# Performance work log

Measured on AMD Instinct MI355X. Metric: run time of the kernel, lower is better.

## Reference

```python
import jax, jax.numpy as jnp
import numpy as np
from jax import lax

# static config (matches init_kwargs / input_specs)
B, T, DUR = 16, 256, 4
MEL = T * DUR                      # 1024 frames; durations rows each sum to MEL
D, H, DH, L = 512, 8, 64, 4
INTER, K, OUT = 2048, 3, 80
VOCAB, MAXLEN = 256, 4096


def _sincos(maxlen, d):
    den = jnp.exp(-jnp.arange(0, d, 2).astype(jnp.float32) * (np.log(10000.0) / d))
    ang = jnp.arange(maxlen, dtype=jnp.float32)[:, None] * den[None, :]
    return jnp.stack([jnp.sin(ang), jnp.cos(ang)], axis=-1).reshape(maxlen, d)


def _ln(x, g, b):
    m = jnp.mean(x, -1, keepdims=True)
    v = jnp.mean((x - m) ** 2, -1, keepdims=True)
    return (x - m) * lax.rsqrt(v + 1e-5) * g + b


def _layer(x, am, wqkv, bqkv, wo, bo, ln1g, ln1b, c1w, c1b, c2w, c2b, ln2g, ln2b):
    bs, s, _ = x.shape
    qkv = (x @ wqkv + bqkv).reshape(bs, s, 3, H, DH)
    q, k, v = qkv[:, :, 0], qkv[:, :, 1], qkv[:, :, 2]
    scores = jnp.einsum('bqhd,bkhd->bhqk', q, k) / np.sqrt(DH).astype(np.float32)
    scores = scores + am[:, None, None, :]          # additive key mask (-inf padded)
    attn = jax.nn.softmax(scores, axis=-1)
    ctx = jnp.einsum('bhqk,bkhd->bqhd', attn, v).reshape(bs, s, H * DH)
    x = _ln(x + ctx @ wo + bo, ln1g, ln1b)
    h = lax.conv_general_dilated(x, c1w, (1,), 'SAME', dimension_numbers=('NLC', 'LIO', 'NLC')) + c1b
    h = jax.nn.relu(h)
    h = lax.conv_general_dilated(h, c2w, (1,), 'SAME', dimension_numbers=('NLC', 'LIO', 'NLC')) + c2b
    return _ln(x + h, ln2g, ln2b)


def _stack(x, am, params):
    for i in range(L):
        x = _layer(x, am, *(p[i] for p in params))
    return x


def setup_inputs() -> dict:
    key = jax.random.key(0)
    ks = iter(jax.random.split(key, 64))

    def nrm(shape, s=0.02):
        return jax.random.normal(next(ks), shape, jnp.float32) * s

    inp = {
        'tokens': jax.random.randint(next(ks), (B, T), 0, VOCAB),
        'token_lengths': jax.random.randint(next(ks), (B,), T // 2, T),
        'melspec_length': jax.random.randint(next(ks), (B,), MEL // 2, MEL),
        'durations': jnp.full((B, T), DUR, jnp.int32),   # rows sum to MEL (module assert)
        'mel_len': MEL,
        'emb': nrm((VOCAB, D), 1.0),
    }
    for pre in ('enc', 'dec'):
        inp[pre + '_wqkv'] = nrm((L, D, 3 * H * DH))
        inp[pre + '_bqkv'] = jnp.zeros((L, 3 * H * DH))
        inp[pre + '_wo'] = nrm((L, H * DH, D))
        inp[pre + '_bo'] = jnp.zeros((L, D))
        inp[pre + '_ln1g'] = jnp.ones((L, D))
        inp[pre + '_ln1b'] = jnp.zeros((L, D))
        inp[pre + '_c1w'] = nrm((L, K, D, INTER))
        inp[pre + '_c1b'] = jnp.zeros((L, INTER))
        inp[pre + '_c2w'] = nrm((L, K, INTER, D))
        inp[pre + '_c2b'] = jnp.zeros((L, D))
        inp[pre + '_ln2g'] = jnp.ones((L, D))
        inp[pre + '_ln2b'] = jnp.zeros((L, D))
    inp['out_w'] = nrm((D, OUT))
    inp['out_b'] = jnp.zeros((OUT,))
    return inp


def reference(tokens, token_lengths, melspec_length, durations, mel_len, emb,
              enc_wqkv, enc_bqkv, enc_wo, enc_bo, enc_ln1g, enc_ln1b,
              enc_c1w, enc_c1b, enc_c2w, enc_c2b, enc_ln2g, enc_ln2b,
              dec_wqkv, dec_bqkv, dec_wo, dec_bo, dec_ln1g, dec_ln1b,
              dec_c1w, dec_c1b, dec_c2w, dec_c2b, dec_ln2g, dec_ln2b,
              out_w, out_b):
    bs, t = tokens.shape
    pos = _sincos(MAXLEAN := MAXLEN, D)
    x = emb[tokens]
    # faithful to original: x + (x + pos_embedding[:bs]) where pos buffer is [maxlen,1,D]
    x = 2.0 * x + pos[:bs][:, None, :]
    am = jnp.where(jnp.arange(t)[None, :] > token_lengths[:, None], -jnp.inf, 0.0)
    enc = _stack(x, am, (enc_wqkv, enc_bqkv, enc_wo, enc_bo, enc_ln1g, enc_ln1b,
                         enc_c1w, enc_c1b, enc_c2w, enc_c2b, enc_ln2g, enc_ln2b))
    # length regulator: equivalent gather form of mask.T @ encoder (O(MEL*D) not O(T*MEL*D))
    cums = jnp.cumsum(durations, axis=1)
    frames = jnp.arange(mel_len)
    idx = jax.vmap(lambda c: jnp.searchsorted(c, frames, side='right'))(cums)  # [B, MEL]
    dec_in = jnp.take_along_axis(enc, idx[:, :, None], axis=1)
    keep = (frames[None, :] <= melspec_length[:, None]).astype(dec_in.dtype)
    dec_in = dec_in * keep[:, :, None]
    am2 = jnp.where(frames[None, :] > melspec_length[:, None], -jnp.inf, 0.0)
    dec = _stack(dec_in, am2, (dec_wqkv, dec_bqkv, dec_wo, dec_bo, dec_ln1g, dec_ln1b,
                               dec_c1w, dec_c1b, dec_c2w, dec_c2b, dec_ln2g, dec_ln2b))
    out = dec @ out_w + out_b                      # [B, MEL, OUT]
    return jnp.transpose(out, (0, 2, 1))           # [B, OUT, MEL]
```

## Files before the change

### kernel.cpp

```cpp
#include <hip/hip_runtime.h>

typedef unsigned short u16;
typedef short short8 __attribute__((ext_vector_type(8)));
typedef float floatx4 __attribute__((ext_vector_type(4)));

static constexpr int CB = 16, CT = 256, CMEL = 1024, CD = 512, CH = 8, CDH = 64, CL = 4;
static constexpr int CINTER = 2048, COUT = 80;
static constexpr int CQKV = 3 * CH * CDH;

static __device__ __forceinline__ float bf2f(u16 u) {
  union { unsigned u; float f; } v; v.u = ((unsigned)u) << 16; return v.f;
}
static __device__ __forceinline__ u16 f2bf(float f) {
  union { float f; unsigned u; } v; v.f = f;
  unsigned r = v.u + 0x7fffu + ((v.u >> 16) & 1u);
  return (u16)(r >> 16);
}

static __device__ __forceinline__ void gld16(const u16* g, u16* lds) {
  __builtin_amdgcn_global_load_lds((const __attribute__((address_space(1))) void*)g,
                                   (__attribute__((address_space(3))) void*)lds, 16, 0, 0);
}

template<int NT, bool RELU>
__global__ __launch_bounds__(256)
void gemm2_k(const u16* __restrict__ A, const u16* __restrict__ Bm,
             u16* __restrict__ Cm, const float* __restrict__ bias,
             int M, int N, int K, int lda, int ldb, int ldc,
             int Sm1, long tapStrideB, const u16* __restrict__ zp)
{
  constexpr int BM = 128, BN = 128;
  constexpr int H = (NT == 3) ? 8 : 0;
  constexpr int AR = BM + 2 * H;
  __shared__ u16 As[AR * 32];
  __shared__ u16 Bs[NT * BN * 32];

  const int t = threadIdx.x;
  const int lane = t & 63;
  const int wave = t >> 6;
  const int wrow = wave >> 1;
  const int wcol = wave & 1;
  const int bn0 = blockIdx.x * BN;
  const int bm0 = blockIdx.y * BM;

  floatx4 acc[4][4];
#pragma unroll
  for (int i = 0; i < 4; ++i)
#pragma unroll
    for (int j = 0; j < 4; ++j) acc[i][j] = (floatx4){0.f, 0.f, 0.f, 0.f};

  const int rsub = lane >> 2;
  const int g8 = (((lane & 3) ^ ((lane >> 3) & 3)) << 3);

  const u16* aP0; const u16* aP1; const u16* aP2 = nullptr;
  {
    int gg0 = bm0 - H + wave * 16 + rsub;
    int gg1 = bm0 - H + (wave + 4) * 16 + rsub;
    aP0 = ((NT == 1) || ((unsigned)gg0 < (unsigned)M)) ? A + (long)gg0 * lda + g8 : nullptr;
    aP1 = ((NT == 1) || ((unsigned)gg1 < (unsigned)M)) ? A + (long)gg1 * lda + g8 : nullptr;
    if (NT == 3 && wave == 0) {
      int gg2 = bm0 - H + 128 + rsub;
      aP2 = ((unsigned)gg2 < (unsigned)M) ? A + (long)gg2 * lda + g8 : nullptr;
    }
  }
  const int aL0 = wave * 512, aL1 = (wave + 4) * 512, aL2 = 8 * 512;

  const u16* bP[NT][2]; int bL[NT][2];
#pragma unroll
  for (int i = 0; i < NT; ++i)
#pragma unroll
    for (int j = 0; j < 2; ++j) {
      int r = (wave + j * 4) * 16 + rsub;
      bP[i][j] = Bm + (long)i * tapStrideB + (long)(bn0 + r) * ldb + g8;
      bL[i][j] = (i * BN + (wave + j * 4) * 16) * 32;
    }

  const int q = lane >> 4, fm = lane & 15;
  const int swzB = (q ^ ((fm >> 1) & 3)) << 3;
  int swzA[NT];
  bool mv[NT][4];
#pragma unroll
  for (int tap = 0; tap < NT; ++tap) {
    const int dlt = tap - ((NT == 3) ? 1 : 0);
    swzA[tap] = (q ^ ((((H + dlt + fm) & 15) >> 1) & 3)) << 3;
#pragma unroll
    for (int i = 0; i < 4; ++i) {
      int s = (bm0 + wrow * 64 + i * 16 + fm) & Sm1;
      mv[tap][i] = ((unsigned)(s + dlt) <= (unsigned)Sm1);
    }
  }
  const short8 zero8 = {};

  for (int k0 = 0; k0 < K; k0 += 32) {
    gld16(aP0 ? aP0 + k0 : zp, &As[aL0]);
    gld16(aP1 ? aP1 + k0 : zp, &As[aL1]);
    if (NT == 3 && wave == 0) gld16(aP2 ? aP2 + k0 : zp, &As[aL2]);
#pragma unroll
    for (int i = 0; i < NT; ++i)
#pragma unroll
      for (int j = 0; j < 2; ++j) gld16(bP[i][j] + k0, &Bs[bL[i][j]]);
    __syncthreads();

#pragma unroll
    for (int tap = 0; tap < NT; ++tap) {
      const int dlt = tap - ((NT == 3) ? 1 : 0);
      short8 af[4], bfr[4];
#pragma unroll
      for (int i = 0; i < 4; ++i) {
        af[i] = *(const short8*)&As[(wrow * 64 + i * 16 + fm + H + dlt) * 32 + swzA[tap]];
        if (NT == 3 && !mv[tap][i]) af[i] = zero8;
      }
#pragma unroll
      for (int j = 0; j < 4; ++j)
        bfr[j] = *(const short8*)&Bs[(tap * BN + wcol * 64 + j * 16 + fm) * 32 + swzB];
#pragma unroll
      for (int i = 0; i < 4; ++i)
#pragma unroll
        for (int j = 0; j < 4; ++j)
          acc[i][j] = __builtin_amdgcn_mfma_f32_16x16x32_bf16(af[i], bfr[j], acc[i][j], 0, 0, 0);
    }
    __syncthreads();
  }

  const int rbase = bm0 + wrow * 64 + ((lane >> 4) << 2);
  const int cbase = bn0 + wcol * 64 + fm;
#pragma unroll
  for (int j = 0; j < 4; ++j) {
    int col = cbase + j * 16;
    float bv = bias ? bias[col] : 0.f;
#pragma unroll
    for (int i = 0; i < 4; ++i) {
#pragma unroll
      for (int r = 0; r < 4; ++r) {
        int row = rbase + i * 16 + r;
        float v = acc[i][j][r] + bv;
        if (RELU) v = fmaxf(v, 0.f);
        Cm[(long)row * ldc + col] = f2bf(v);
      }
    }
  }
}

__global__ __launch_bounds__(512)
void attn_k(const u16* __restrict__ qkv, const u16* __restrict__ vt,
            u16* __restrict__ ctx, const int* __restrict__ lens, int S)
{
  __shared__ __attribute__((aligned(16))) u16 Ks[2][128 * 32];
  __shared__ __attribute__((aligned(16))) u16 Vts[4][64 * 32];
  __shared__ __attribute__((aligned(16))) u16 Ps[8][16][136];

  const int t = threadIdx.x, lane = t & 63, w = t >> 6;
  const int bh = blockIdx.y, b = bh >> 3, h = bh & 7;
  const int q0 = blockIdx.x * 128;
  const int len = lens[b];
  const int fm = lane & 15, quad = lane >> 4;
  const int swz8 = ((quad ^ ((fm >> 1) & 3)) << 3);
  const int rsub = lane >> 2;
  const int g8 = (((lane & 3) ^ ((lane >> 3) & 3)) << 3);

  const int qrow = q0 + w * 16 + fm;
  short8 bq[2];
  bq[0] = *(const short8*)&qkv[(long)(b * S + qrow) * CQKV + h * 64 + quad * 8];
  bq[1] = *(const short8*)&qkv[(long)(b * S + qrow) * CQKV + h * 64 + 32 + quad * 8];

  const int ksW = w & 1, rgA = w >> 1, rgB = (w >> 1) + 4;
  const u16* kBaseA = qkv + ((long)b * S + rgA * 16 + rsub) * CQKV + CD + h * 64 + ksW * 32 + g8;
  const u16* kBaseB = qkv + ((long)b * S + rgB * 16 + rsub) * CQKV + CD + h * 64 + ksW * 32 + g8;
  u16* kDstA = &Ks[ksW][rgA * 512];
  u16* kDstB = &Ks[ksW][rgB * 512];
  const int kvs0 = (2 * w) >> 2, dhc0 = (2 * w) & 3;
  const int kvs1 = (2 * w + 1) >> 2, dhc1 = (2 * w + 1) & 3;
  const u16* vBase0 = vt + ((long)bh * 64 + dhc0 * 16 + rsub) * S + kvs0 * 32 + g8;
  const u16* vBase1 = vt + ((long)bh * 64 + dhc1 * 16 + rsub) * S + kvs1 * 32 + g8;
  u16* vDst0 = &Vts[kvs0][dhc0 * 512];
  u16* vDst1 = &Vts[kvs1][dhc1 * 512];

  floatx4 acc_o[4];
#pragma unroll
  for (int j = 0; j < 4; ++j) acc_o[j] = (floatx4){0.f, 0.f, 0.f, 0.f};
  float m = -1e30f, l = 0.f;

  for (int kv0 = 0; kv0 < S; kv0 += 128) {
    __syncthreads();
    gld16(kBaseA + (long)kv0 * CQKV, kDstA);
    gld16(kBaseB + (long)kv0 * CQKV, kDstB);
    gld16(vBase0 + kv0, vDst0);
    gld16(vBase1 + kv0, vDst1);
    __syncthreads();

    floatx4 sa[8];
#pragma unroll
    for (int i = 0; i < 8; ++i) sa[i] = (floatx4){0.f, 0.f, 0.f, 0.f};
#pragma unroll
    for (int ks = 0; ks < 2; ++ks) {
#pragma unroll
      for (int mi = 0; mi < 8; ++mi) {
        short8 ak = *(const short8*)&Ks[ks][(mi * 16 + fm) * 32 + swz8];
        sa[mi] = __builtin_amdgcn_mfma_f32_16x16x32_bf16(ak, bq[ks], sa[mi], 0, 0, 0);
      }
    }

    float p[8][4], tm = -1e30f;
#pragma unroll
    for (int mi = 0; mi < 8; ++mi)
#pragma unroll
      for (int r = 0; r < 4; ++r) {
        int kvg = kv0 + mi * 16 + quad * 4 + r;
        float v = (kvg <= len) ? sa[mi][r] * 0.125f : -1e30f;
        p[mi][r] = v; tm = fmaxf(tm, v);
      }
    tm = fmaxf(tm, __shfl_xor(tm, 16));
    tm = fmaxf(tm, __shfl_xor(tm, 32));
    const float mnew = fmaxf(m, tm);
    const float al = __expf(m - mnew);
    float ts = 0.f;
#pragma unroll
    for (int mi = 0; mi < 8; ++mi)
#pragma unroll
      for (int r = 0; r < 4; ++r) { float e = __expf(p[mi][r] - mnew); p[mi][r] = e; ts += e; }
    ts += __shfl_xor(ts, 16);
    ts += __shfl_xor(ts, 32);
    l = l * al + ts; m = mnew;
    float al4[4];
#pragma unroll
    for (int r = 0; r < 4; ++r) al4[r] = __shfl(al, ((lane >> 4) << 2) + r, 64);
#pragma unroll
    for (int j = 0; j < 4; ++j)
#pragma unroll
      for (int r = 0; r < 4; ++r) acc_o[j][r] *= al4[r];

#pragma unroll
    for (int mi = 0; mi < 8; ++mi) {
      unsigned u01 = (unsigned)f2bf(p[mi][0]) | ((unsigned)f2bf(p[mi][1]) << 16);
      unsigned u23 = (unsigned)f2bf(p[mi][2]) | ((unsigned)f2bf(p[mi][3]) << 16);
      *(uint2*)&Ps[w][fm][mi * 16 + quad * 4] = make_uint2(u01, u23);
    }

#pragma unroll
    for (int kvs = 0; kvs < 4; ++kvs) {
      short8 ap = *(const short8*)&Ps[w][fm][kvs * 32 + quad * 8];
#pragma unroll
      for (int nj = 0; nj < 4; ++nj) {
        short8 bv = *(const short8*)&Vts[kvs][(nj * 16 + fm) * 32 + swz8];
        acc_o[nj] = __builtin_amdgcn_mfma_f32_16x16x32_bf16(ap, bv, acc_o[nj], 0, 0, 0);
      }
    }
  }

  float li4[4];
#pragma unroll
  for (int r = 0; r < 4; ++r) li4[r] = 1.f / __shfl(l, ((lane >> 4) << 2) + r, 64);
#pragma unroll
  for (int nj = 0; nj < 4; ++nj)
#pragma unroll
    for (int r = 0; r < 4; ++r) {
      int qr = q0 + w * 16 + quad * 4 + r;
      ctx[(long)(b * S + qr) * CD + h * 64 + nj * 16 + fm] = f2bf(acc_o[nj][r] * li4[r]);
    }
}

template<int BM, int BN>
__global__ __launch_bounds__(256)
void gemmF_k(const u16* __restrict__ A, const u16* __restrict__ Bm,
             float* __restrict__ Cm, const float* __restrict__ bias,
             int M, int N, int K, int lda, int ldb,
             const u16* __restrict__ zp)
{
  __shared__ u16 As[BM * 32];
  __shared__ u16 Bs[BN * 32];

  const int t = threadIdx.x;
  const int lane = t & 63;
  const int wave = t >> 6;
  constexpr int WCOLS = BN / 64;
  const int wrow = wave / WCOLS;
  const int wcol = wave % WCOLS;
  const int bn0 = blockIdx.x * BN;
  const int bm0 = blockIdx.y * BM;

  floatx4 acc[4][4];
#pragma unroll
  for (int i = 0; i < 4; ++i)
#pragma unroll
    for (int j = 0; j < 4; ++j) acc[i][j] = (floatx4){0.f, 0.f, 0.f, 0.f};

  const int rsub = lane >> 2;
  const int g8 = (((lane & 3) ^ ((lane >> 3) & 3)) << 3);
  constexpr int PA = BM / 64, PB = BN / 64;

  const int q = lane >> 4, fm = lane & 15;
  const int swz8 = ((q ^ ((fm >> 1) & 3)) << 3);

  const u16* aP[PA]; const u16* bP[PB];
#pragma unroll
  for (int p = 0; p < PA; ++p)
    aP[p] = A + (long)(bm0 + p * 64 + wave * 16 + rsub) * lda + g8;
#pragma unroll
  for (int p = 0; p < PB; ++p) {
    int r = p * 64 + wave * 16 + rsub;
    bP[p] = ((bn0 + r) < N) ? (Bm + (long)(bn0 + r) * ldb + g8) : nullptr;
  }

  for (int k0 = 0; k0 < K; k0 += 32) {
#pragma unroll
    for (int p = 0; p < PA; ++p)
      gld16(aP[p] + k0, &As[(p * 64 + wave * 16) * 32]);
#pragma unroll
    for (int p = 0; p < PB; ++p)
      gld16(bP[p] ? bP[p] + k0 : zp, &Bs[(p * 64 + wave * 16) * 32]);
    __syncthreads();

    short8 af[4], bfr[4];
#pragma unroll
    for (int i = 0; i < 4; ++i)
      af[i] = *(const short8*)&As[(wrow * 64 + i * 16 + fm) * 32 + swz8];
#pragma unroll
    for (int j = 0; j < 4; ++j)
      bfr[j] = *(const short8*)&Bs[(wcol * 64 + j * 16 + fm) * 32 + swz8];
#pragma unroll
    for (int i = 0; i < 4; ++i)
#pragma unroll
      for (int j = 0; j < 4; ++j)
        acc[i][j] = __builtin_amdgcn_mfma_f32_16x16x32_bf16(af[i], bfr[j], acc[i][j], 0, 0, 0);
    __syncthreads();
  }

  const int rbase = bm0 + wrow * 64 + ((lane >> 4) << 2);
  const int cbase = bn0 + wcol * 64 + (lane & 15);
#pragma unroll
  for (int j = 0; j < 4; ++j) {
    int col = cbase + j * 16;
    if (col >= N) continue;
    float bv = bias ? bias[col] : 0.f;
#pragma unroll
    for (int i = 0; i < 4; ++i) {
#pragma unroll
      for (int r = 0; r < 4; ++r) {
        int row = rbase + i * 16 + r;
        Cm[((long)(row >> 10) * COUT + col) * CMEL + (row & 1023)] = acc[i][j][r] + bv;
      }
    }
  }
}

__global__ void cvt_t_k(const float* __restrict__ src, u16* __restrict__ dst, int K, int N)
{
  const int tap = blockIdx.z;
  const int n0 = blockIdx.x * 32, k0 = blockIdx.y * 32;
  __shared__ float tile[32][33];
  const int t = threadIdx.x;
  const int c = t & 31, rr = t >> 5;
  const float* s = src + (long)tap * K * N;
  u16* d = dst + (long)tap * K * N;
#pragma unroll
  for (int i = 0; i < 4; ++i) {
    int k = k0 + rr + i * 8, n = n0 + c;
    tile[rr + i * 8][c] = (k < K && n < N) ? s[(long)k * N + n] : 0.f;
  }
  __syncthreads();
#pragma unroll
  for (int i = 0; i < 4; ++i) {
    int n = n0 + rr + i * 8, k = k0 + c;
    if (n < N && k < K) d[(long)n * K + k] = f2bf(tile[c][rr + i * 8]);
  }
}

__global__ void vtr_k(const u16* __restrict__ qkv, u16* __restrict__ vt, int S)
{
  const int s0 = blockIdx.x * 64;
  const int bh = blockIdx.y;
  const int b = bh >> 3, h = bh & 7;
  __shared__ u16 tile[64][65];
  const int t = threadIdx.x;
  const int wave = t >> 6, lane = t & 63;
#pragma unroll
  for (int i = 0; i < 16; ++i) {
    int sl = wave * 16 + i;
    tile[sl][lane] = qkv[(long)(b * S + s0 + sl) * CQKV + 2 * CD + h * 64 + lane];
  }
  __syncthreads();
  const int dl = t >> 2, sc4 = (t & 3) << 4;
  u16* dstp = vt + ((long)bh * 64 + dl) * S + s0 + sc4;
  short8 v0, v1;
#pragma unroll
  for (int j = 0; j < 8; ++j) { v0[j] = (short)tile[sc4 + j][dl]; v1[j] = (short)tile[sc4 + 8 + j][dl]; }
  *(short8*)dstp = v0;
  *(short8*)(dstp + 8) = v1;
}

__global__ void fill_k(float* __restrict__ o, int n, float v)
{
  int i = blockIdx.x * 256 + threadIdx.x;
  if (i < n) o[i] = v;
}

__global__ void embed_k(const int* __restrict__ tok, const float* __restrict__ emb,
                        u16* __restrict__ X)
{
  const long idx = (long)blockIdx.x * 256 + threadIdx.x;
  const int d = (int)(idx & (CD - 1));
  const int m = (int)(idx >> 9);
  const int b = m >> 8;
  const float e = emb[(long)tok[m] * CD + d];
  const int i2 = d >> 1;
  const float den = __expf(-(float)(2 * i2) * (9.210340371976184f / 512.f));
  const float ang = (float)b * den;
  const float p = (d & 1) ? __cosf(ang) : __sinf(ang);
  X[idx] = f2bf(2.f * e + p);
}

__global__ __launch_bounds__(256)
void ln_res_k(const u16* __restrict__ X, const u16* __restrict__ Y,
              const float* __restrict__ g, const float* __restrict__ bta,
              u16* __restrict__ O)
{
  const int w = threadIdx.x >> 6, lane = threadIdx.x & 63;
  const long m = (long)blockIdx.x * 4 + w;
  const long base = m * CD + lane * 8;
  const short8 xv = *(const short8*)&X[base];
  const short8 yv = *(const short8*)&Y[base];
  float v[8]; float s = 0.f;
#pragma unroll
  for (int j = 0; j < 8; ++j) { v[j] = bf2f((u16)xv[j]) + bf2f((u16)yv[j]); s += v[j]; }
#pragma unroll
  for (int o = 1; o < 64; o <<= 1) s += __shfl_xor(s, o);
  const float mean = s * (1.f / 512.f);
  float qs = 0.f;
#pragma unroll
  for (int j = 0; j < 8; ++j) { v[j] -= mean; qs += v[j] * v[j]; }
#pragma unroll
  for (int o = 1; o < 64; o <<= 1) qs += __shfl_xor(qs, o);
  const float rstd = rsqrtf(qs * (1.f / 512.f) + 1e-5f);
  const float4 g0 = *(const float4*)&g[lane * 8];
  const float4 g1 = *(const float4*)&g[lane * 8 + 4];
  const float4 b0 = *(const float4*)&bta[lane * 8];
  const float4 b1 = *(const float4*)&bta[lane * 8 + 4];
  short8 ov;
  ov[0] = (short)f2bf(v[0] * rstd * g0.x + b0.x);
  ov[1] = (short)f2bf(v[1] * rstd * g0.y + b0.y);
  ov[2] = (short)f2bf(v[2] * rstd * g0.z + b0.z);
  ov[3] = (short)f2bf(v[3] * rstd * g0.w + b0.w);
  ov[4] = (short)f2bf(v[4] * rstd * g1.x + b1.x);
  ov[5] = (short)f2bf(v[5] * rstd * g1.y + b1.y);
  ov[6] = (short)f2bf(v[6] * rstd * g1.z + b1.z);
  ov[7] = (short)f2bf(v[7] * rstd * g1.w + b1.w);
  *(short8*)&O[base] = ov;
}

__global__ void cumsum_k(const int* __restrict__ dur, int* __restrict__ cums)
{
  int b = threadIdx.x;
  if (b < CB) {
    int s = 0;
    for (int t = 0; t < CT; ++t) { s += dur[b * CT + t]; cums[b * CT + t] = s; }
  }
}

__global__ __launch_bounds__(256)
void regulate_k(const u16* __restrict__ xe, const int* __restrict__ cums,
                const int* __restrict__ mlen, u16* __restrict__ xd)
{
  const int w = threadIdx.x >> 6, lane = threadIdx.x & 63;
  const int m = blockIdx.x * 4 + w;
  const int b = m >> 10, f = m & (CMEL - 1);
  int lo = 0, hi = CT;
  while (lo < hi) { int mid = (lo + hi) >> 1; if (cums[b * CT + mid] <= f) lo = mid + 1; else hi = mid; }
  const int idx = min(lo, CT - 1);
  const bool keep = (f <= mlen[b]);
  short8 val = {};
  if (keep) val = *(const short8*)&xe[((long)b * CT + idx) * CD + lane * 8];
  *(short8*)&xd[(long)m * CD + lane * 8] = val;
}

extern "C" void kernel_launch(void* const* d_in, const int* in_sizes, int n_in,
                              void* d_out, int out_size, void* d_ws, size_t ws_size,
                              hipStream_t stream)
{
  (void)in_sizes; (void)n_in;
  const int*   tokens = (const int*)d_in[0];
  const int*   tlen   = (const int*)d_in[1];
  const int*   mlen   = (const int*)d_in[2];
  const int*   dur    = (const int*)d_in[3];
  const float* emb    = (const float*)d_in[5];
  const float* ew[12]; const float* dw[12];
  for (int i = 0; i < 12; ++i) { ew[i] = (const float*)d_in[6 + i]; dw[i] = (const float*)d_in[18 + i]; }
  const float* out_w = (const float*)d_in[30];
  const float* out_b = (const float*)d_in[31];

  const int Me = CB * CT;
  const int Md = CB * CMEL;

  const size_t SZ_ZP   = 256;
  const size_t SZ_WBUF = (size_t)3 * CD * CINTER * 2;
  const size_t SZ_XE   = (size_t)Me * CD * 2;
  const size_t SZ_XD   = (size_t)Md * CD * 2;
  const size_t SZ_QKV  = (size_t)Md * CQKV * 2;
  const size_t SZ_HB   = (size_t)Md * CINTER * 2;
  const size_t SZ_CUMS = (size_t)CB * CT * 4;
  auto al = [](size_t b) { return (b + 255) & ~(size_t)255; };
  size_t U = al(SZ_QKV) > al(SZ_HB) ? al(SZ_QKV) : al(SZ_HB);
  size_t total = al(SZ_ZP) + al(SZ_WBUF) + al(SZ_XE) + 3 * al(SZ_XD) + U + al(SZ_CUMS);
  if (total > ws_size) {
    fill_k<<<dim3((unsigned)((out_size + 255) / 256)), dim3(256), 0, stream>>>(
        (float*)d_out, out_size, 1000.0f);
    return;
  }

  char* p = (char*)d_ws;
  auto take = [&](size_t bytes) { char* r = p; p += al(bytes); return r; };
  u16*  zp   = (u16*)take(SZ_ZP);
  u16*  wbuf = (u16*)take(SZ_WBUF);
  u16*  xe   = (u16*)take(SZ_XE);
  u16*  xd   = (u16*)take(SZ_XD);
  u16*  x1   = (u16*)take(SZ_XD);
  u16*  yb   = (u16*)take(SZ_XD);
  char* U0   = take(U);
  u16*  qkvB = (u16*)U0;
  u16*  hb   = (u16*)U0;
  int* cums = (int*)take(SZ_CUMS);

  hipMemsetAsync(zp, 0, SZ_ZP, stream);

  auto cvtT = [&](const float* s, u16* d, int K, int N, int taps) {
    cvt_t_k<<<dim3((unsigned)((N + 31) / 32), (unsigned)((K + 31) / 32), (unsigned)taps),
              dim3(256), 0, stream>>>(s, d, K, N);
  };

  embed_k<<<dim3((unsigned)((long)Me * CD / 256)), dim3(256), 0, stream>>>(tokens, emb, xe);

  auto run_stack = [&](u16* x, int S, int M, const int* lens, const float* const* W) {
    u16* vt = yb;
    for (int l = 0; l < CL; ++l) {
      cvtT(W[0] + (long)l * CD * CQKV, wbuf, CD, CQKV, 1);
      gemm2_k<1, false><<<dim3(CQKV / 128, M / 128), dim3(256), 0, stream>>>(
          x, wbuf, qkvB, W[1] + l * CQKV, M, CQKV, CD, CD, CD, CQKV, S - 1, 0, zp);
      vtr_k<<<dim3((unsigned)(S / 64), (unsigned)(CB * CH)), dim3(256), 0, stream>>>(qkvB, vt, S);
      attn_k<<<dim3((unsigned)(S / 128), (unsigned)(CB * CH)), dim3(512), 0, stream>>>(
          qkvB, vt, x1, lens, S);
      cvtT(W[2] + (long)l * CD * CD, wbuf, CD, CD, 1);
      gemm2_k<1, false><<<dim3(CD / 128, M / 128), dim3(256), 0, stream>>>(
          x1, wbuf, yb, W[3] + l * CD, M, CD, CD, CD, CD, CD, S - 1, 0, zp);
      ln_res_k<<<dim3((unsigned)(M / 4)), dim3(256), 0, stream>>>(
          x, yb, W[4] + l * CD, W[5] + l * CD, x1);
      cvtT(W[6] + (long)l * 3 * CD * CINTER, wbuf, CD, CINTER, 3);
      gemm2_k<3, true><<<dim3(CINTER / 128, M / 128), dim3(256), 0, stream>>>(
          x1, wbuf, hb, W[7] + l * CINTER, M, CINTER, CD, CD, CD, CINTER,
          S - 1, (long)CD * CINTER, zp);
      cvtT(W[8] + (long)l * 3 * CINTER * CD, wbuf, CINTER, CD, 3);
      gemm2_k<3, false><<<dim3(CD / 128, M / 128), dim3(256), 0, stream>>>(
          hb, wbuf, yb, W[9] + l * CD, M, CD, CINTER, CINTER, CINTER, CD,
          S - 1, (long)CINTER * CD, zp);
      ln_res_k<<<dim3((unsigned)(M / 4)), dim3(256), 0, stream>>>(
          x1, yb, W[10] + l * CD, W[11] + l * CD, x);
    }
  };

  run_stack(xe, CT, Me, tlen, ew);

  cumsum_k<<<dim3(1), dim3(64), 0, stream>>>(dur, cums);
  regulate_k<<<dim3((unsigned)(CB * CMEL / 4)), dim3(256), 0, stream>>>(xe, cums, mlen, xd);

  run_stack(xd, CMEL, Md, mlen, dw);

  cvtT(out_w, wbuf, CD, COUT, 1);
  gemmF_k<128, 128><<<dim3(1, Md / 128), dim3(256), 0, stream>>>(
      xd, wbuf, (float*)d_out, out_b, Md, COUT, CD, CD, CD, zp);
}
```

Before: 2.621 ms.

## Add BM=64 GEMM tiles for small encoder GEMMs and skip masked KV blocks

Templates the GEMM on the M-tile size and uses 64-row tiles for the N=512 projection and conv2 GEMMs in the encoder stack (M=4096), doubling the block count so more compute units are occupied. Separately, attention now stops its KV loop after the last 128-key block that holds unmasked keys, based on the per-batch length, skipping blocks that would be fully masked. Smaller tiles lower per-block data reuse, and the early exit depends on masked keys contributing exactly zero.

```diff
diff --git a/kernel.cpp b/kernel.cpp
--- a/kernel.cpp
+++ b/kernel.cpp
@@ -22,16 +22,18 @@
                                    (__attribute__((address_space(3))) void*)lds, 16, 0, 0);
 }
 
-template<int NT, bool RELU>
+template<int BMT, int NT, bool RELU>
 __global__ __launch_bounds__(256)
 void gemm2_k(const u16* __restrict__ A, const u16* __restrict__ Bm,
              u16* __restrict__ Cm, const float* __restrict__ bias,
              int M, int N, int K, int lda, int ldb, int ldc,
              int Sm1, long tapStrideB, const u16* __restrict__ zp)
 {
-  constexpr int BM = 128, BN = 128;
+  constexpr int BM = BMT, BN = 128;
   constexpr int H = (NT == 3) ? 8 : 0;
   constexpr int AR = BM + 2 * H;
+  constexpr int ACH = AR / 16;
+  constexpr int FR = BM / 32;
   __shared__ u16 As[AR * 32];
   __shared__ u16 Bs[NT * BN * 32];
 
@@ -43,27 +45,27 @@
   const int bn0 = blockIdx.x * BN;
   const int bm0 = blockIdx.y * BM;
 
-  floatx4 acc[4][4];
-#pragma unroll
-  for (int i = 0; i < 4; ++i)
+  floatx4 acc[FR][4];
+#pragma unroll
+  for (int i = 0; i < FR; ++i)
 #pragma unroll
     for (int j = 0; j < 4; ++j) acc[i][j] = (floatx4){0.f, 0.f, 0.f, 0.f};
 
   const int rsub = lane >> 2;
   const int g8 = (((lane & 3) ^ ((lane >> 3) & 3)) << 3);
 
-  const u16* aP0; const u16* aP1; const u16* aP2 = nullptr;
-  {
-    int gg0 = bm0 - H + wave * 16 + rsub;
-    int gg1 = bm0 - H + (wave + 4) * 16 + rsub;
-    aP0 = ((NT == 1) || ((unsigned)gg0 < (unsigned)M)) ? A + (long)gg0 * lda + g8 : nullptr;
-    aP1 = ((NT == 1) || ((unsigned)gg1 < (unsigned)M)) ? A + (long)gg1 * lda + g8 : nullptr;
-    if (NT == 3 && wave == 0) {
-      int gg2 = bm0 - H + 128 + rsub;
-      aP2 = ((unsigned)gg2 < (unsigned)M) ? A + (long)gg2 * lda + g8 : nullptr;
-    }
-  }
-  const int aL0 = wave * 512, aL1 = (wave + 4) * 512, aL2 = 8 * 512;
+  const u16* aP[3]; int aL[3]; bool aU[3];
+#pragma unroll
+  for (int s = 0; s < 3; ++s) {
+    const int c = wave + 4 * s;
+    aU[s] = (c < ACH);
+    aL[s] = c * 512;
+    aP[s] = nullptr;
+    if (aU[s]) {
+      int gg = bm0 - H + c * 16 + rsub;
+      aP[s] = ((NT == 1) || ((unsigned)gg < (unsigned)M)) ? A + (long)gg * lda + g8 : nullptr;
+    }
+  }
 
   const u16* bP[NT][2]; int bL[NT][2];
 #pragma unroll
@@ -78,23 +80,23 @@
   const int q = lane >> 4, fm = lane & 15;
   const int swzB = (q ^ ((fm >> 1) & 3)) << 3;
   int swzA[NT];
-  bool mv[NT][4];
+  bool mv[NT][FR];
 #pragma unroll
   for (int tap = 0; tap < NT; ++tap) {
     const int dlt = tap - ((NT == 3) ? 1 : 0);
     swzA[tap] = (q ^ ((((H + dlt + fm) & 15) >> 1) & 3)) << 3;
 #pragma unroll
-    for (int i = 0; i < 4; ++i) {
-      int s = (bm0 + wrow * 64 + i * 16 + fm) & Sm1;
+    for (int i = 0; i < FR; ++i) {
+      int s = (bm0 + wrow * (BM / 2) + i * 16 + fm) & Sm1;
       mv[tap][i] = ((unsigned)(s + dlt) <= (unsigned)Sm1);
     }
   }
   const short8 zero8 = {};
 
   for (int k0 = 0; k0 < K; k0 += 32) {
-    gld16(aP0 ? aP0 + k0 : zp, &As[aL0]);
-    gld16(aP1 ? aP1 + k0 : zp, &As[aL1]);
-    if (NT == 3 && wave == 0) gld16(aP2 ? aP2 + k0 : zp, &As[aL2]);
+#pragma unroll
+    for (int s = 0; s < 3; ++s)
+      if (aU[s]) gld16(aP[s] ? aP[s] + k0 : zp, &As[aL[s]]);
 #pragma unroll
     for (int i = 0; i < NT; ++i)
 #pragma unroll
@@ -104,17 +106,17 @@
 #pragma unroll
     for (int tap = 0; tap < NT; ++tap) {
       const int dlt = tap - ((NT == 3) ? 1 : 0);
-      short8 af[4], bfr[4];
-#pragma unroll
-      for (int i = 0; i < 4; ++i) {
-        af[i] = *(const short8*)&As[(wrow * 64 + i * 16 + fm + H + dlt) * 32 + swzA[tap]];
+      short8 af[FR], bfr[4];
+#pragma unroll
+      for (int i = 0; i < FR; ++i) {
+        af[i] = *(const short8*)&As[(wrow * (BM / 2) + i * 16 + fm + H + dlt) * 32 + swzA[tap]];
         if (NT == 3 && !mv[tap][i]) af[i] = zero8;
       }
 #pragma unroll
       for (int j = 0; j < 4; ++j)
         bfr[j] = *(const short8*)&Bs[(tap * BN + wcol * 64 + j * 16 + fm) * 32 + swzB];
 #pragma unroll
-      for (int i = 0; i < 4; ++i)
+      for (int i = 0; i < FR; ++i)
 #pragma unroll
         for (int j = 0; j < 4; ++j)
           acc[i][j] = __builtin_amdgcn_mfma_f32_16x16x32_bf16(af[i], bfr[j], acc[i][j], 0, 0, 0);
@@ -122,14 +124,14 @@
     __syncthreads();
   }
 
-  const int rbase = bm0 + wrow * 64 + ((lane >> 4) << 2);
+  const int rbase = bm0 + wrow * (BM / 2) + ((lane >> 4) << 2);
   const int cbase = bn0 + wcol * 64 + fm;
 #pragma unroll
   for (int j = 0; j < 4; ++j) {
     int col = cbase + j * 16;
     float bv = bias ? bias[col] : 0.f;
 #pragma unroll
-    for (int i = 0; i < 4; ++i) {
+    for (int i = 0; i < FR; ++i) {
 #pragma unroll
       for (int r = 0; r < 4; ++r) {
         int row = rbase + i * 16 + r;
@@ -180,7 +182,8 @@
   for (int j = 0; j < 4; ++j) acc_o[j] = (floatx4){0.f, 0.f, 0.f, 0.f};
   float m = -1e30f, l = 0.f;
 
-  for (int kv0 = 0; kv0 < S; kv0 += 128) {
+  const int nkv = min(S, ((len >> 7) + 1) << 7);
+  for (int kv0 = 0; kv0 < nkv; kv0 += 128) {
     __syncthreads();
     gld16(kBaseA + (long)kv0 * CQKV, kDstA);
     gld16(kBaseB + (long)kv0 * CQKV, kDstB);
@@ -530,26 +533,36 @@
 
   auto run_stack = [&](u16* x, int S, int M, const int* lens, const float* const* W) {
     u16* vt = yb;
+    const bool small = (M < 8192);
     for (int l = 0; l < CL; ++l) {
       cvtT(W[0] + (long)l * CD * CQKV, wbuf, CD, CQKV, 1);
-      gemm2_k<1, false><<<dim3(CQKV / 128, M / 128), dim3(256), 0, stream>>>(
+      gemm2_k<128, 1, false><<<dim3(CQKV / 128, M / 128), dim3(256), 0, stream>>>(
           x, wbuf, qkvB, W[1] + l * CQKV, M, CQKV, CD, CD, CD, CQKV, S - 1, 0, zp);
       vtr_k<<<dim3((unsigned)(S / 64), (unsigned)(CB * CH)), dim3(256), 0, stream>>>(qkvB, vt, S);
       attn_k<<<dim3((unsigned)(S / 128), (unsigned)(CB * CH)), dim3(512), 0, stream>>>(
           qkvB, vt, x1, lens, S);
       cvtT(W[2] + (long)l * CD * CD, wbuf, CD, CD, 1);
-      gemm2_k<1, false><<<dim3(CD / 128, M / 128), dim3(256), 0, stream>>>(
-          x1, wbuf, yb, W[3] + l * CD, M, CD, CD, CD, CD, CD, S - 1, 0, zp);
+      if (small)
+        gemm2_k<64, 1, false><<<dim3(CD / 128, M / 64), dim3(256), 0, stream>>>(
+            x1, wbuf, yb, W[3] + l * CD, M, CD, CD, CD, CD, CD, S - 1, 0, zp);
+      else
+        gemm2_k<128, 1, false><<<dim3(CD / 128, M / 128), dim3(256), 0, stream>>>(
+            x1, wbuf, yb, W[3] + l * CD, M, CD, CD, CD, CD, CD, S - 1, 0, zp);
       ln_res_k<<<dim3((unsigned)(M / 4)), dim3(256), 0, stream>>>(
           x, yb, W[4] + l * CD, W[5] + l * CD, x1);
       cvtT(W[6] + (long)l * 3 * CD * CINTER, wbuf, CD, CINTER, 3);
-      gemm2_k<3, true><<<dim3(CINTER / 128, M / 128), dim3(256), 0, stream>>>(
+      gemm2_k<128, 3, true><<<dim3(CINTER / 128, M / 128), dim3(256), 0, stream>>>(
           x1, wbuf, hb, W[7] + l * CINTER, M, CINTER, CD, CD, CD, CINTER,
           S - 1, (long)CD * CINTER, zp);
       cvtT(W[8] + (long)l * 3 * CINTER * CD, wbuf, CINTER, CD, 3);
-      gemm2_k<3, false><<<dim3(CD / 128, M / 128), dim3(256), 0, stream>>>(
-          hb, wbuf, yb, W[9] + l * CD, M, CD, CINTER, CINTER, CINTER, CD,
-          S - 1, (long)CINTER * CD, zp);
+      if (small)
+        gemm2_k<64, 3, false><<<dim3(CD / 128, M / 64), dim3(256), 0, stream>>>(
+            hb, wbuf, yb, W[9] + l * CD, M, CD, CINTER, CINTER, CINTER, CD,
+            S - 1, (long)CINTER * CD, zp);
+      else
+        gemm2_k<128, 3, false><<<dim3(CD / 128, M / 128), dim3(256), 0, stream>>>(
+            hb, wbuf, yb, W[9] + l * CD, M, CD, CINTER, CINTER, CINTER, CD,
+            S - 1, (long)CINTER * CD, zp);
       ln_res_k<<<dim3((unsigned)(M / 4)), dim3(256), 0, stream>>>(
           x1, yb, W[10] + l * CD, W[11] + l * CD, x);
     }
```

Result: faster. 2.494 ms (-4.8%).
